# Optimization experiments

Measured on AMD Instinct MI355X. Metric: run time of the kernel, lower is better.

## Reference

```python
import jax, jax.numpy as jnp
import numpy as np

D_MODEL = 1024
HEADS = 16
D_K = D_MODEL // HEADS
D_FF = 4096
EPS = 1e-5


def _layernorm(x, gamma, beta):
    mu = jnp.mean(x, axis=-1, keepdims=True)
    var = jnp.var(x, axis=-1, keepdims=True)
    return (x - mu) * jax.lax.rsqrt(var + EPS) * gamma + beta


def setup_inputs() -> dict:
    key = jax.random.key(0)
    ks = jax.random.split(key, 8)
    s = 0.02
    return {
        "x": jax.random.normal(ks[0], (4, 2048, D_MODEL), dtype=jnp.float32),
        "wq": jax.random.normal(ks[1], (D_MODEL, D_MODEL), dtype=jnp.float32) * s,
        "wk": jax.random.normal(ks[2], (D_MODEL, D_MODEL), dtype=jnp.float32) * s,
        "wv": jax.random.normal(ks[3], (D_MODEL, D_MODEL), dtype=jnp.float32) * s,
        "wo": jax.random.normal(ks[4], (D_MODEL, D_MODEL), dtype=jnp.float32) * s,
        "w1": jax.random.normal(ks[5], (D_MODEL, D_FF), dtype=jnp.float32) * s,
        "b1": jnp.zeros((D_FF,), dtype=jnp.float32),
        "w2": jax.random.normal(ks[6], (D_FF, D_MODEL), dtype=jnp.float32) * s,
        "b2": jnp.zeros((D_MODEL,), dtype=jnp.float32),
        "g1": jnp.ones((D_MODEL,), dtype=jnp.float32),
        "be1": jnp.zeros((D_MODEL,), dtype=jnp.float32),
        "g2": jnp.ones((D_MODEL,), dtype=jnp.float32),
        "be2": jnp.zeros((D_MODEL,), dtype=jnp.float32),
    }


def reference(x, wq, wk, wv, wo, w1, b1, w2, b2, g1, be1, g2, be2):
    B, S, D = x.shape
    # --- multi-head self-attention (dropout = identity at eval) ---
    q = (x @ wq).reshape(B, S, HEADS, D_K).transpose(0, 2, 1, 3)  # [B,H,S,dk]
    k = (x @ wk).reshape(B, S, HEADS, D_K).transpose(0, 2, 1, 3)
    v = (x @ wv).reshape(B, S, HEADS, D_K).transpose(0, 2, 1, 3)
    scores = jnp.einsum("bhqd,bhkd->bhqk", q, k) / jnp.sqrt(jnp.float32(D_K))
    attn = jax.nn.softmax(scores, axis=-1)
    ctx = jnp.einsum("bhqk,bhkd->bhqd", attn, v)
    ctx = ctx.transpose(0, 2, 1, 3).reshape(B, S, D)
    attn_out = ctx @ wo
    # --- add & norm 1 ---
    h = _layernorm(x + attn_out, g1, be1)
    # --- FFN ---
    ffn = jax.nn.relu(h @ w1 + b1) @ w2 + b2
    # --- add & norm 2 ---
    return _layernorm(h + ffn, g2, be2)
```

## Files before the change

### kernel.cpp

```cpp
#include <hip/hip_runtime.h>
#include <hip/hip_bf16.h>


typedef float  floatx2  __attribute__((ext_vector_type(2)));
typedef float  floatx4  __attribute__((ext_vector_type(4)));
typedef float  floatx16 __attribute__((ext_vector_type(16)));
typedef short  shortx8  __attribute__((ext_vector_type(8)));
typedef short  shortx4  __attribute__((ext_vector_type(4)));
typedef int    intx4    __attribute__((ext_vector_type(4)));
typedef unsigned uintx2 __attribute__((ext_vector_type(2)));

__device__ __forceinline__ short f2bs(float f) {
    union { float f; unsigned u; } a; a.f = f;
    unsigned r = a.u + 0x7fffu + ((a.u >> 16) & 1u);
    return (short)(r >> 16);
}

__device__ __forceinline__ float fexp2(float x) {
#if __has_builtin(__builtin_amdgcn_exp2f)
    return __builtin_amdgcn_exp2f(x);
#else
    return __expf(0.6931471805599453f * x);
#endif
}

__device__ __forceinline__ void lane32swap(unsigned& a, unsigned& b) {
#if __has_builtin(__builtin_amdgcn_permlane32_swap)
    uintx2 r = __builtin_amdgcn_permlane32_swap(a, b, false, false);
    a = r[0]; b = r[1];
#else
    int hl = (threadIdx.x & 63) >> 5;
    unsigned ta = (unsigned)__shfl_xor((int)a, 32);
    unsigned tb = (unsigned)__shfl_xor((int)b, 32);
    unsigned na = hl ? tb : a;
    unsigned nb = hl ? b : ta;
    a = na; b = nb;
#endif
}

__device__ __forceinline__ void gload16(const short* g, short* l) {
    __builtin_amdgcn_global_load_lds(
        (const __attribute__((address_space(1))) void*)g,
        (__attribute__((address_space(3))) void*)l,
        16, 0, 0);
}

#define WAITV(n) asm volatile("s_waitcnt vmcnt(" #n ")" ::: "memory")
#define FENCE    asm volatile("" ::: "memory")

__device__ __forceinline__ void trans_tile(const float* __restrict__ in,
                                           short* __restrict__ out,
                                           int N, int K, int k0, int n0,
                                           short (*t)[68]) {
    const int tid = threadIdx.x;
    const int r = tid >> 4, c4 = (tid & 15) * 4;
#pragma unroll
    for (int i = 0; i < 4; ++i) {
        int k = r + i * 16;
        floatx4 v = *(const floatx4*)(in + (size_t)(k0 + k) * N + n0 + c4);
        shortx4 s;
#pragma unroll
        for (int j = 0; j < 4; ++j) s[j] = f2bs(v[j]);
        *(shortx4*)(&t[k][c4]) = s;
    }
    __syncthreads();
#pragma unroll
    for (int i = 0; i < 4; ++i) {
        int n = r + i * 16;
        shortx4 s;
#pragma unroll
        for (int j = 0; j < 4; ++j) s[j] = t[c4 + j][n];
        *(shortx4*)(out + (size_t)(n0 + n) * K + k0 + c4) = s;
    }
}

__global__ __launch_bounds__(256) void prep_kernel(
    const float* __restrict__ wq, const float* __restrict__ wk,
    const float* __restrict__ wv, const float* __restrict__ wo,
    const float* __restrict__ w1, const float* __restrict__ w2,
    const float* __restrict__ x,
    short* wqt, short* wkt, short* wvt, short* wot,
    short* w1t, short* w2t, short* xb)
{
    __shared__ __align__(16) short t[64][68];
    const int bid = blockIdx.x;
    if (bid < 1024) {
        const int widx = bid >> 8, local = bid & 255;
        const float* in = widx == 0 ? wq : widx == 1 ? wk : widx == 2 ? wv : wo;
        short* out = widx == 0 ? wqt : widx == 1 ? wkt : widx == 2 ? wvt : wot;
        trans_tile(in, out, 1024, 1024, (local & 15) * 64, (local >> 4) * 64, t);
    } else if (bid < 2048) {
        const int local = bid - 1024;
        trans_tile(w1, w1t, 4096, 1024, (local & 15) * 64, (local >> 4) * 64, t);
    } else if (bid < 3072) {
        const int local = bid - 2048;
        trans_tile(w2, w2t, 1024, 4096, (local & 63) * 64, (local >> 6) * 64, t);
    } else {
        const int local = bid - 3072;
#pragma unroll
        for (int j = 0; j < 4; ++j) {
            int i = local * 1024 + j * 256 + threadIdx.x;
            floatx4 v = *(const floatx4*)(x + (size_t)i * 4);
            shortx4 o;
            o[0] = f2bs(v[0]); o[1] = f2bs(v[1]); o[2] = f2bs(v[2]); o[3] = f2bs(v[3]);
            *(shortx4*)(xb + (size_t)i * 4) = o;
        }
    }
}

template<int EPI, int BN>
__global__ __launch_bounds__(512, 2) void gemm256(
    const short* __restrict__ A, const short* __restrict__ Bt, const int K, const int N,
    short* __restrict__ outb, float* __restrict__ outf,
    const float* __restrict__ bias, const float* __restrict__ resf)
{
    constexpr int BUFSZ = 16384 + BN * 64;
    constexpr int NF = BN / 64;
    __shared__ __align__(16) short Ls[2 * BUFSZ];
    const int tid = threadIdx.x;
    const int w = tid >> 6, lane = tid & 63;
    const int quad = lane >> 4, l16 = lane & 15;
    const int wm = w >> 2, wn = w & 3;
    const int bx = blockIdx.x, by = blockIdx.y;

    const int srow = w * 16 + (lane >> 3);
    const int uc0 = ((lane & 7) ^ ((lane >> 4) & 7)) * 8;
    const int uc1 = ((lane & 7) ^ (((lane >> 4) + 4) & 7)) * 8;
    const short* aS0 = A  + (size_t)(by * 256 + srow) * K + uc0;
    const short* aS1 = A  + (size_t)(by * 256 + srow + 8) * K + uc1;
    const short* bS0 = Bt + (size_t)(bx * BN + srow) * K + uc0;
    const short* bS1 = Bt + (size_t)(bx * BN + srow + 8) * K + uc1;
    const size_t hK = (size_t)128 * K;
    const int wsl = w * 1024;

    const int rswz = (l16 >> 1) & 7;
    const int ru0 = (quad ^ rswz) * 8;
    const int ru1 = ((4 + quad) ^ rswz) * 8;
    const int aRd = (wm * 64 + l16) * 64;
    const int bRd = (wn * 32 + l16) * 64;

    floatx4 acc[8][NF] = {};
    shortx8 af[4][2], blo[2][2], bhi[2][2];

#define S_A0(buf, kc) { short* p = Ls + (buf) * BUFSZ + wsl;         gload16(aS0 + (kc), p);      gload16(aS1 + (kc), p + 512);      FENCE; }
#define S_A1(buf, kc) { short* p = Ls + (buf) * BUFSZ + 8192 + wsl;  gload16(aS0 + hK + (kc), p); gload16(aS1 + hK + (kc), p + 512); FENCE; }
#define S_B0(buf, kc) { short* p = Ls + (buf) * BUFSZ + 16384 + wsl; gload16(bS0 + (kc), p);      gload16(bS1 + (kc), p + 512);      FENCE; }
#define S_B1(buf, kc) { short* p = Ls + (buf) * BUFSZ + 24576 + wsl; gload16(bS0 + hK + (kc), p); gload16(bS1 + hK + (kc), p + 512); FENCE; }
#define MF(a, b, c) c = __builtin_amdgcn_mfma_f32_16x16x32_bf16(a, b, c, 0, 0, 0)

    const int NT = K >> 6;

    if constexpr (BN == 256) {
        S_A0(0, 0) S_B0(0, 0) S_B1(0, 0) S_A1(0, 0)
        for (int t = 0; t < NT - 1; ++t) {
            const int rb = t & 1, wbuf = rb ^ 1, kc = (t + 1) * 64;
            const short* Ab = Ls + rb * BUFSZ;
            const short* Bb = Ab + 16384;
            WAITV(4); __builtin_amdgcn_s_barrier(); FENCE;
#pragma unroll
            for (int mf = 0; mf < 4; ++mf) {
                af[mf][0] = *(const shortx8*)(Ab + aRd + mf * 1024 + ru0);
                af[mf][1] = *(const shortx8*)(Ab + aRd + mf * 1024 + ru1);
            }
#pragma unroll
            for (int nf = 0; nf < 2; ++nf) {
                blo[nf][0] = *(const shortx8*)(Bb + bRd + nf * 1024 + ru0);
                blo[nf][1] = *(const shortx8*)(Bb + bRd + nf * 1024 + ru1);
            }
            S_A0(wbuf, kc)
            __builtin_amdgcn_s_setprio(1);
#pragma unroll
            for (int mf = 0; mf < 4; ++mf)
#pragma unroll
                for (int nf = 0; nf < 2; ++nf) {
                    MF(af[mf][0], blo[nf][0], acc[mf][nf]);
                    MF(af[mf][1], blo[nf][1], acc[mf][nf]);
                }
            __builtin_amdgcn_s_setprio(0);
            WAITV(4); __builtin_amdgcn_s_barrier(); FENCE;
#pragma unroll
            for (int nf = 0; nf < 2; ++nf) {
                bhi[nf][0] = *(const shortx8*)(Bb + bRd + 8192 + nf * 1024 + ru0);
                bhi[nf][1] = *(const shortx8*)(Bb + bRd + 8192 + nf * 1024 + ru1);
            }
            S_B0(wbuf, kc)
            __builtin_amdgcn_s_setprio(1);
#pragma unroll
            for (int mf = 0; mf < 4; ++mf)
#pragma unroll
                for (int nf = 0; nf < 2; ++nf) {
                    MF(af[mf][0], bhi[nf][0], acc[mf][2 + nf]);
                    MF(af[mf][1], bhi[nf][1], acc[mf][2 + nf]);
                }
            __builtin_amdgcn_s_setprio(0);
            WAITV(4); __builtin_amdgcn_s_barrier(); FENCE;
#pragma unroll
            for (int mf = 0; mf < 4; ++mf) {
                af[mf][0] = *(const shortx8*)(Ab + aRd + 8192 + mf * 1024 + ru0);
                af[mf][1] = *(const shortx8*)(Ab + aRd + 8192 + mf * 1024 + ru1);
            }
            S_B1(wbuf, kc)
            __builtin_amdgcn_s_setprio(1);
#pragma unroll
            for (int mf = 0; mf < 4; ++mf)
#pragma unroll
                for (int nf = 0; nf < 2; ++nf) {
                    MF(af[mf][0], blo[nf][0], acc[4 + mf][nf]);
                    MF(af[mf][1], blo[nf][1], acc[4 + mf][nf]);
                }
            __builtin_amdgcn_s_setprio(0);
            S_A1(wbuf, kc)
            __builtin_amdgcn_s_setprio(1);
#pragma unroll
            for (int mf = 0; mf < 4; ++mf)
#pragma unroll
                for (int nf = 0; nf < 2; ++nf) {
                    MF(af[mf][0], bhi[nf][0], acc[4 + mf][2 + nf]);
                    MF(af[mf][1], bhi[nf][1], acc[4 + mf][2 + nf]);
                }
            __builtin_amdgcn_s_setprio(0);
        }
        {
            const int rb = (NT - 1) & 1;
            const short* Ab = Ls + rb * BUFSZ;
            const short* Bb = Ab + 16384;
            WAITV(4); __builtin_amdgcn_s_barrier(); FENCE;
#pragma unroll
            for (int mf = 0; mf < 4; ++mf) {
                af[mf][0] = *(const shortx8*)(Ab + aRd + mf * 1024 + ru0);
                af[mf][1] = *(const shortx8*)(Ab + aRd + mf * 1024 + ru1);
            }
#pragma unroll
            for (int nf = 0; nf < 2; ++nf) {
                blo[nf][0] = *(const shortx8*)(Bb + bRd + nf * 1024 + ru0);
                blo[nf][1] = *(const shortx8*)(Bb + bRd + nf * 1024 + ru1);
            }
            __builtin_amdgcn_s_setprio(1);
#pragma unroll
            for (int mf = 0; mf < 4; ++mf)
#pragma unroll
                for (int nf = 0; nf < 2; ++nf) {
                    MF(af[mf][0], blo[nf][0], acc[mf][nf]);
                    MF(af[mf][1], blo[nf][1], acc[mf][nf]);
                }
            __builtin_amdgcn_s_setprio(0);
            WAITV(2); __builtin_amdgcn_s_barrier(); FENCE;
#pragma unroll
            for (int nf = 0; nf < 2; ++nf) {
                bhi[nf][0] = *(const shortx8*)(Bb + bRd + 8192 + nf * 1024 + ru0);
                bhi[nf][1] = *(const shortx8*)(Bb + bRd + 8192 + nf * 1024 + ru1);
            }
            __builtin_amdgcn_s_setprio(1);
#pragma unroll
            for (int mf = 0; mf < 4; ++mf)
#pragma unroll
                for (int nf = 0; nf < 2; ++nf) {
                    MF(af[mf][0], bhi[nf][0], acc[mf][2 + nf]);
                    MF(af[mf][1], bhi[nf][1], acc[mf][2 + nf]);
                }
            __builtin_amdgcn_s_setprio(0);
            WAITV(0); __builtin_amdgcn_s_barrier(); FENCE;
#pragma unroll
            for (int mf = 0; mf < 4; ++mf) {
                af[mf][0] = *(const shortx8*)(Ab + aRd + 8192 + mf * 1024 + ru0);
                af[mf][1] = *(const shortx8*)(Ab + aRd + 8192 + mf * 1024 + ru1);
            }
            __builtin_amdgcn_s_setprio(1);
#pragma unroll
            for (int mf = 0; mf < 4; ++mf)
#pragma unroll
                for (int nf = 0; nf < 2; ++nf) {
                    MF(af[mf][0], blo[nf][0], acc[4 + mf][nf]);
                    MF(af[mf][1], blo[nf][1], acc[4 + mf][nf]);
                    MF(af[mf][0], bhi[nf][0], acc[4 + mf][2 + nf]);
                    MF(af[mf][1], bhi[nf][1], acc[4 + mf][2 + nf]);
                }
            __builtin_amdgcn_s_setprio(0);
        }
    } else {
        S_A0(0, 0) S_B0(0, 0) S_A1(0, 0)
        for (int t = 0; t < NT - 1; ++t) {
            const int rb = t & 1, wbuf = rb ^ 1, kc = (t + 1) * 64;
            const short* Ab = Ls + rb * BUFSZ;
            const short* Bb = Ab + 16384;
            WAITV(2); __builtin_amdgcn_s_barrier(); FENCE;
#pragma unroll
            for (int mf = 0; mf < 4; ++mf) {
                af[mf][0] = *(const shortx8*)(Ab + aRd + mf * 1024 + ru0);
                af[mf][1] = *(const shortx8*)(Ab + aRd + mf * 1024 + ru1);
            }
#pragma unroll
            for (int nf = 0; nf < 2; ++nf) {
                blo[nf][0] = *(const shortx8*)(Bb + bRd + nf * 1024 + ru0);
                blo[nf][1] = *(const shortx8*)(Bb + bRd + nf * 1024 + ru1);
            }
            S_A0(wbuf, kc)
            __builtin_amdgcn_s_setprio(1);
#pragma unroll
            for (int mf = 0; mf < 4; ++mf)
#pragma unroll
                for (int nf = 0; nf < 2; ++nf) {
                    MF(af[mf][0], blo[nf][0], acc[mf][nf]);
                    MF(af[mf][1], blo[nf][1], acc[mf][nf]);
                }
            __builtin_amdgcn_s_setprio(0);
            WAITV(2); __builtin_amdgcn_s_barrier(); FENCE;
#pragma unroll
            for (int mf = 0; mf < 4; ++mf) {
                af[mf][0] = *(const shortx8*)(Ab + aRd + 8192 + mf * 1024 + ru0);
                af[mf][1] = *(const shortx8*)(Ab + aRd + 8192 + mf * 1024 + ru1);
            }
            S_B0(wbuf, kc) S_A1(wbuf, kc)
            __builtin_amdgcn_s_setprio(1);
#pragma unroll
            for (int mf = 0; mf < 4; ++mf)
#pragma unroll
                for (int nf = 0; nf < 2; ++nf) {
                    MF(af[mf][0], blo[nf][0], acc[4 + mf][nf]);
                    MF(af[mf][1], blo[nf][1], acc[4 + mf][nf]);
                }
            __builtin_amdgcn_s_setprio(0);
        }
        {
            const int rb = (NT - 1) & 1;
            const short* Ab = Ls + rb * BUFSZ;
            const short* Bb = Ab + 16384;
            WAITV(2); __builtin_amdgcn_s_barrier(); FENCE;
#pragma unroll
            for (int mf = 0; mf < 4; ++mf) {
                af[mf][0] = *(const shortx8*)(Ab + aRd + mf * 1024 + ru0);
                af[mf][1] = *(const shortx8*)(Ab + aRd + mf * 1024 + ru1);
            }
#pragma unroll
            for (int nf = 0; nf < 2; ++nf) {
                blo[nf][0] = *(const shortx8*)(Bb + bRd + nf * 1024 + ru0);
                blo[nf][1] = *(const shortx8*)(Bb + bRd + nf * 1024 + ru1);
            }
            __builtin_amdgcn_s_setprio(1);
#pragma unroll
            for (int mf = 0; mf < 4; ++mf)
#pragma unroll
                for (int nf = 0; nf < 2; ++nf) {
                    MF(af[mf][0], blo[nf][0], acc[mf][nf]);
                    MF(af[mf][1], blo[nf][1], acc[mf][nf]);
                }
            __builtin_amdgcn_s_setprio(0);
            WAITV(0); __builtin_amdgcn_s_barrier(); FENCE;
#pragma unroll
            for (int mf = 0; mf < 4; ++mf) {
                af[mf][0] = *(const shortx8*)(Ab + aRd + 8192 + mf * 1024 + ru0);
                af[mf][1] = *(const shortx8*)(Ab + aRd + 8192 + mf * 1024 + ru1);
            }
            __builtin_amdgcn_s_setprio(1);
#pragma unroll
            for (int mf = 0; mf < 4; ++mf)
#pragma unroll
                for (int nf = 0; nf < 2; ++nf) {
                    MF(af[mf][0], blo[nf][0], acc[4 + mf][nf]);
                    MF(af[mf][1], blo[nf][1], acc[4 + mf][nf]);
                }
            __builtin_amdgcn_s_setprio(0);
        }
    }

#pragma unroll
    for (int mf = 0; mf < 8; ++mf) {
        const int grow0 = by * 256 + (mf >> 2) * 128 + wm * 64 + (mf & 3) * 16 + quad * 4;
#pragma unroll
        for (int nf = 0; nf < NF; ++nf) {
            int gcol;
            if constexpr (BN == 256)
                gcol = bx * 256 + (nf >> 1) * 128 + wn * 32 + (nf & 1) * 16 + l16;
            else
                gcol = bx * 128 + wn * 32 + nf * 16 + l16;
            const floatx4 a = acc[mf][nf];
            if constexpr (EPI == 5) {
                const int slice = gcol >> 10, c = gcol & 1023;
                const int hh = c >> 6, d = c & 63;
                const int b = grow0 >> 11, s0 = grow0 & 2047;
                if (slice == 2) {
                    short* vt = outb + ((size_t)16 << 20);
                    shortx4 pkv;
#pragma unroll
                    for (int r = 0; r < 4; ++r) pkv[r] = f2bs(a[r]);
                    *(shortx4*)(vt + ((size_t)((b * 16 + hh) * 64 + d)) * 2048 + s0) = pkv;
                } else {
                    short* dst = slice ? (outb + ((size_t)8 << 20)) : outb;
                    float sc = slice ? 1.f : 0.125f * 1.4426950408889634f;
#pragma unroll
                    for (int r = 0; r < 4; ++r)
                        dst[(((size_t)(b * 16 + hh)) * 2048 + (s0 + r)) * 64 + d] =
                            f2bs(a[r] * sc);
                }
            } else if constexpr (EPI == 1) {
                const float bv = bias[gcol];
#pragma unroll
                for (int r = 0; r < 4; ++r) {
                    float v = fmaxf(a[r] + bv, 0.f);
                    outb[(size_t)(grow0 + r) * N + gcol] = f2bs(v);
                }
            } else if constexpr (EPI == 2) {
#pragma unroll
                for (int r = 0; r < 4; ++r)
                    outf[(size_t)(grow0 + r) * N + gcol] =
                        a[r] + resf[(size_t)(grow0 + r) * N + gcol];
            } else if constexpr (EPI == 3) {
                const float bv = bias[gcol];
#pragma unroll
                for (int r = 0; r < 4; ++r)
                    outf[(size_t)(grow0 + r) * N + gcol] =
                        a[r] + bv + resf[(size_t)(grow0 + r) * N + gcol];
            }
        }
    }
#undef S_A0
#undef S_A1
#undef S_B0
#undef S_B1
#undef MF
}

__global__ __launch_bounds__(256) void ln_kernel(
    const float* __restrict__ in, float* __restrict__ outf, short* __restrict__ outb,
    const float* __restrict__ g, const float* __restrict__ be, int writeB)
{
    __shared__ float red[8];
    const int row = blockIdx.x, tid = threadIdx.x;
    const float* p = in + (size_t)row * 1024;
    floatx4 v = *(const floatx4*)(p + tid * 4);
    float s = v[0] + v[1] + v[2] + v[3];
    float q = v[0] * v[0] + v[1] * v[1] + v[2] * v[2] + v[3] * v[3];
#pragma unroll
    for (int off = 32; off; off >>= 1) {
        s += __shfl_xor(s, off);
        q += __shfl_xor(q, off);
    }
    int w = tid >> 6, lane = tid & 63;
    if (lane == 0) { red[w] = s; red[4 + w] = q; }
    __syncthreads();
    s = red[0] + red[1] + red[2] + red[3];
    q = red[4] + red[5] + red[6] + red[7];
    float mean = s * (1.f / 1024.f);
    float var = q * (1.f / 1024.f) - mean * mean;
    float rs = rsqrtf(var + 1e-5f);
    floatx4 gv = *(const floatx4*)(g + tid * 4);
    floatx4 bv = *(const floatx4*)(be + tid * 4);
    floatx4 o4;
#pragma unroll
    for (int i = 0; i < 4; ++i) o4[i] = (v[i] - mean) * rs * gv[i] + bv[i];
    *(floatx4*)(outf + (size_t)row * 1024 + tid * 4) = o4;
    if (writeB) {
        shortx4 ob;
#pragma unroll
        for (int i = 0; i < 4; ++i) ob[i] = f2bs(o4[i]);
        *(shortx4*)(outb + (size_t)row * 1024 + tid * 4) = ob;
    }
}

__global__ __launch_bounds__(256) void attn_kernel(
    const short* __restrict__ Q, const short* __restrict__ K,
    const short* __restrict__ Vt, short* __restrict__ ctx)
{
    __shared__ __align__(16) short Ks[128 * 72];
    __shared__ __align__(16) short Vs[64 * 136];
    const int tid = threadIdx.x;
    const int q0 = blockIdx.x * 128, bh = blockIdx.y;
    const int w = tid >> 6, lane = tid & 63, l31 = lane & 31, hl = lane >> 5;
    const size_t sb = (size_t)bh * 2048 * 64;

    shortx8 qf[4];
#pragma unroll
    for (int ks = 0; ks < 4; ++ks)
        qf[ks] = *(const shortx8*)(Q + sb + (size_t)(q0 + w * 32 + l31) * 64 + ks * 16 + hl * 8);

    const int krow = tid >> 3, kcol = (tid & 7) * 8;
    const int vrow = tid >> 4, vcol = (tid & 15) * 8;

    floatx16 o[2] = {};
    floatx2 rsA = {0.f, 0.f}, rsB = {0.f, 0.f};
    const floatx16 z = {};

    intx4 kv[4], vv[4];
#pragma unroll
    for (int i = 0; i < 4; ++i) {
        kv[i] = *(const intx4*)(K + sb + (size_t)(i * 32 + krow) * 64 + kcol);
        vv[i] = *(const intx4*)(Vt + sb + (size_t)(i * 16 + vrow) * 2048 + vcol);
    }

#define LD_AK(mt, ks) (*(const shortx8*)(Ks + ((mt) * 32 + l31) * 72 + (ks) * 16 + hl * 8))
#define LD_AV(mtd, mt, ksl) (*(const shortx8*)(Vs + ((mtd) * 32 + l31) * 136 + (mt) * 32 + (ksl) * 16 + hl * 8))

    for (int kt = 0; kt < 16; ++kt) {
        __syncthreads();
#pragma unroll
        for (int i = 0; i < 4; ++i) {
            *(intx4*)(Ks + (i * 32 + krow) * 72 + kcol) = kv[i];
            *(intx4*)(Vs + (i * 16 + vrow) * 136 + vcol) = vv[i];
        }
        __syncthreads();
        if (kt < 15) {
            const int kv0 = (kt + 1) * 128;
#pragma unroll
            for (int i = 0; i < 4; ++i) {
                kv[i] = *(const intx4*)(K + sb + (size_t)(kv0 + i * 32 + krow) * 64 + kcol);
                vv[i] = *(const intx4*)(Vt + sb + (size_t)(i * 16 + vrow) * 2048 + kv0 + vcol);
            }
        }

        floatx16 sc;
        {
            __builtin_amdgcn_s_setprio(1);
            sc = __builtin_amdgcn_mfma_f32_32x32x16_bf16(LD_AK(0, 0), qf[0], z, 0, 0, 0);
            sc = __builtin_amdgcn_mfma_f32_32x32x16_bf16(LD_AK(0, 1), qf[1], sc, 0, 0, 0);
            sc = __builtin_amdgcn_mfma_f32_32x32x16_bf16(LD_AK(0, 2), qf[2], sc, 0, 0, 0);
            sc = __builtin_amdgcn_mfma_f32_32x32x16_bf16(LD_AK(0, 3), qf[3], sc, 0, 0, 0);
            __builtin_amdgcn_s_setprio(0);
        }
#pragma unroll
        for (int mt = 0; mt < 4; ++mt) {
            floatx16 sn;
            if (mt < 3) {
                __builtin_amdgcn_s_setprio(1);
                sn = __builtin_amdgcn_mfma_f32_32x32x16_bf16(LD_AK(mt + 1, 0), qf[0], z, 0, 0, 0);
                sn = __builtin_amdgcn_mfma_f32_32x32x16_bf16(LD_AK(mt + 1, 1), qf[1], sn, 0, 0, 0);
                sn = __builtin_amdgcn_mfma_f32_32x32x16_bf16(LD_AK(mt + 1, 2), qf[2], sn, 0, 0, 0);
                sn = __builtin_amdgcn_mfma_f32_32x32x16_bf16(LD_AK(mt + 1, 3), qf[3], sn, 0, 0, 0);
                __builtin_amdgcn_s_setprio(0);
            }
            floatx2 ps2[8];
#pragma unroll
            for (int i = 0; i < 8; ++i) {
                ps2[i][0] = fexp2(sc[2 * i]);
                ps2[i][1] = fexp2(sc[2 * i + 1]);
            }
#pragma unroll
            for (int i = 0; i < 8; i += 2) { rsA += ps2[i]; rsB += ps2[i + 1]; }
            unsigned pk[8];
#pragma unroll
            for (int i = 0; i < 8; ++i) {
                union { __hip_bfloat162 h; unsigned u; } cv;
                cv.h = __float22bfloat162_rn(make_float2(ps2[i][0], ps2[i][1]));
                pk[i] = cv.u;
            }
            lane32swap(pk[0], pk[2]);
            lane32swap(pk[1], pk[3]);
            lane32swap(pk[4], pk[6]);
            lane32swap(pk[5], pk[7]);
            __builtin_amdgcn_s_setprio(1);
#pragma unroll
            for (int ksl = 0; ksl < 2; ++ksl) {
                union { unsigned i[4]; shortx8 s8; } fr;
                fr.i[0] = pk[4 * ksl];     fr.i[1] = pk[4 * ksl + 1];
                fr.i[2] = pk[4 * ksl + 2]; fr.i[3] = pk[4 * ksl + 3];
#pragma unroll
                for (int mtd = 0; mtd < 2; ++mtd)
                    o[mtd] = __builtin_amdgcn_mfma_f32_32x32x16_bf16(LD_AV(mtd, mt, ksl), fr.s8, o[mtd], 0, 0, 0);
            }
            __builtin_amdgcn_s_setprio(0);
            if (mt < 3) sc = sn;
        }
    }
#undef LD_AK
#undef LD_AV

    float rsum = rsA[0] + rsA[1] + rsB[0] + rsB[1];
    float tot = rsum + __shfl_xor(rsum, 32);
    float inv = 1.f / tot;

    __syncthreads();
    short* O_lds = Ks;
#pragma unroll
    for (int mtd = 0; mtd < 2; ++mtd)
#pragma unroll
        for (int g = 0; g < 4; ++g) {
            shortx4 p4;
#pragma unroll
            for (int r = 0; r < 4; ++r) p4[r] = f2bs(o[mtd][4 * g + r] * inv);
            *(shortx4*)(O_lds + (w * 32 + l31) * 72 + mtd * 32 + g * 8 + hl * 4) = p4;
        }
    __syncthreads();
    const int b = bh >> 4, head = bh & 15;
#pragma unroll
    for (int it = 0; it < 4; ++it) {
        int idx = it * 256 + tid;
        int q = idx >> 3, ch = idx & 7;
        shortx8 v = *(const shortx8*)(O_lds + q * 72 + ch * 8);
        *(shortx8*)(ctx + ((size_t)(b * 2048 + q0 + q)) * 1024 + head * 64 + ch * 8) = v;
    }
}

extern "C" void kernel_launch(void* const* d_in, const int* in_sizes, int n_in,
                              void* d_out, int out_size, void* d_ws, size_t ws_size,
                              hipStream_t stream) {
    const float* x   = (const float*)d_in[0];
    const float* wq  = (const float*)d_in[1];
    const float* wk  = (const float*)d_in[2];
    const float* wv  = (const float*)d_in[3];
    const float* wo  = (const float*)d_in[4];
    const float* w1  = (const float*)d_in[5];
    const float* b1  = (const float*)d_in[6];
    const float* w2  = (const float*)d_in[7];
    const float* b2  = (const float*)d_in[8];
    const float* g1p = (const float*)d_in[9];
    const float* be1 = (const float*)d_in[10];
    const float* g2p = (const float*)d_in[11];
    const float* be2 = (const float*)d_in[12];
    float* out = (float*)d_out;

    char* ws = (char*)d_ws;
    const size_t MB = 1ull << 20;
    short* wqt  = (short*)(ws + 0 * MB);
    short* wkt  = (short*)(ws + 2 * MB);
    short* wvt  = (short*)(ws + 4 * MB);
    short* wot  = (short*)(ws + 6 * MB);
    short* w1t  = (short*)(ws + 8 * MB);
    short* w2t  = (short*)(ws + 16 * MB);
    short* xb   = (short*)(ws + 24 * MB);
    short* Qb   = (short*)(ws + 40 * MB);
    short* Kb   = (short*)(ws + 56 * MB);
    short* Vtg  = (short*)(ws + 72 * MB);
    short* ctxb = (short*)(ws + 88 * MB);
    float* tf   = (float*)(ws + 104 * MB);
    short* hb   = (short*)(ws + 136 * MB);
    short* f1b  = (short*)(ws + 40 * MB);

    prep_kernel<<<5120, 256, 0, stream>>>(wq, wk, wv, wo, w1, w2, x,
                                          wqt, wkt, wvt, wot, w1t, w2t, xb);

    gemm256<5, 128><<<dim3(24, 32), 512, 0, stream>>>(xb, wqt, 1024, 3072, Qb, nullptr, nullptr, nullptr);
    attn_kernel<<<dim3(16, 64), 256, 0, stream>>>(Qb, Kb, Vtg, ctxb);
    gemm256<2, 128><<<dim3(8, 32), 512, 0, stream>>>(ctxb, wot, 1024, 1024, nullptr, tf, nullptr, x);
    ln_kernel<<<8192, 256, 0, stream>>>(tf, tf, hb, g1p, be1, 1);
    gemm256<1, 256><<<dim3(16, 32), 512, 0, stream>>>(hb, w1t, 1024, 4096, f1b, nullptr, b1, nullptr);
    gemm256<3, 128><<<dim3(8, 32), 512, 0, stream>>>(f1b, w2t, 4096, 1024, nullptr, out, b2, tf);
    ln_kernel<<<8192, 256, 0, stream>>>(out, out, nullptr, g2p, be2, 0);
}
```

Baseline: 410.5 us.

## Load K/V tiles directly to LDS with XOR swizzle in attention kernel

Replaces the register-staged K/V prefetch (global->VGPR->LDS with padded rows) with direct global-to-LDS 16-byte loads (gload16) into unpadded tiles. Bank conflicts are avoided with an XOR swizzle of the column chunk index. The kernel also drops the software-pipelined score MFMA (sn/sc double buffering) and sets launch_bounds min-blocks to 4, which lowers register use to raise occupancy. The cost is that each tile is now loaded synchronously (WAITV(0) before the barrier) with no prefetch overlap. The kernel relies on more resident waves to hide that latency.

```diff
diff --git a/kernel.cpp b/kernel.cpp
--- a/kernel.cpp
+++ b/kernel.cpp
@@ -457,12 +457,13 @@
     }
 }
 
-__global__ __launch_bounds__(256) void attn_kernel(
+__global__ __launch_bounds__(256, 4) void attn_kernel(
     const short* __restrict__ Q, const short* __restrict__ K,
     const short* __restrict__ Vt, short* __restrict__ ctx)
 {
-    __shared__ __align__(16) short Ks[128 * 72];
-    __shared__ __align__(16) short Vs[64 * 136];
+    __shared__ __align__(16) short Ls[16384];
+    short* Ks = Ls;
+    short* Vs = Ls + 8192;
     const int tid = threadIdx.x;
     const int q0 = blockIdx.x * 128, bh = blockIdx.y;
     const int w = tid >> 6, lane = tid & 63, l31 = lane & 31, hl = lane >> 5;
@@ -473,60 +474,45 @@
     for (int ks = 0; ks < 4; ++ks)
         qf[ks] = *(const shortx8*)(Q + sb + (size_t)(q0 + w * 32 + l31) * 64 + ks * 16 + hl * 8);
 
-    const int krow = tid >> 3, kcol = (tid & 7) * 8;
-    const int vrow = tid >> 4, vcol = (tid & 15) * 8;
+    const short* kSrc = K + sb + (size_t)(w * 32 + (lane >> 3)) * 64
+                        + (((lane & 7) ^ ((lane >> 3) & 7)) * 8);
+    int vOff[4];
+#pragma unroll
+    for (int j = 0; j < 4; ++j)
+        vOff[j] = (w * 16 + j * 4 + (lane >> 4)) * 2048
+                  + (((lane & 15) ^ (j * 4 + (lane >> 4))) * 8);
+    const short* vBase = Vt + sb;
+
+    const int kx = l31 & 7, vx = l31 & 15;
 
     floatx16 o[2] = {};
     floatx2 rsA = {0.f, 0.f}, rsB = {0.f, 0.f};
     const floatx16 z = {};
 
-    intx4 kv[4], vv[4];
-#pragma unroll
-    for (int i = 0; i < 4; ++i) {
-        kv[i] = *(const intx4*)(K + sb + (size_t)(i * 32 + krow) * 64 + kcol);
-        vv[i] = *(const intx4*)(Vt + sb + (size_t)(i * 16 + vrow) * 2048 + vcol);
-    }
-
-#define LD_AK(mt, ks) (*(const shortx8*)(Ks + ((mt) * 32 + l31) * 72 + (ks) * 16 + hl * 8))
-#define LD_AV(mtd, mt, ksl) (*(const shortx8*)(Vs + ((mtd) * 32 + l31) * 136 + (mt) * 32 + (ksl) * 16 + hl * 8))
+#define LD_AK(mt, ks) (*(const shortx8*)(Ks + ((mt) * 32 + l31) * 64 + ((((ks) * 2 + hl) ^ kx)) * 8))
+#define LD_AV(mtd, mt, ksl) (*(const shortx8*)(Vs + ((mtd) * 32 + l31) * 128 + ((((mt) * 4 + (ksl) * 2 + hl) ^ vx)) * 8))
 
     for (int kt = 0; kt < 16; ++kt) {
+        const int kv0 = kt * 128;
         __syncthreads();
 #pragma unroll
-        for (int i = 0; i < 4; ++i) {
-            *(intx4*)(Ks + (i * 32 + krow) * 72 + kcol) = kv[i];
-            *(intx4*)(Vs + (i * 16 + vrow) * 136 + vcol) = vv[i];
-        }
+        for (int j = 0; j < 4; ++j)
+            gload16(kSrc + (size_t)kv0 * 64 + j * 512, Ks + (w * 4 + j) * 512);
+#pragma unroll
+        for (int j = 0; j < 4; ++j)
+            gload16(vBase + vOff[j] + kv0, Vs + (w * 4 + j) * 512);
+        WAITV(0);
         __syncthreads();
-        if (kt < 15) {
-            const int kv0 = (kt + 1) * 128;
-#pragma unroll
-            for (int i = 0; i < 4; ++i) {
-                kv[i] = *(const intx4*)(K + sb + (size_t)(kv0 + i * 32 + krow) * 64 + kcol);
-                vv[i] = *(const intx4*)(Vt + sb + (size_t)(i * 16 + vrow) * 2048 + kv0 + vcol);
-            }
-        }
-
-        floatx16 sc;
-        {
-            __builtin_amdgcn_s_setprio(1);
-            sc = __builtin_amdgcn_mfma_f32_32x32x16_bf16(LD_AK(0, 0), qf[0], z, 0, 0, 0);
-            sc = __builtin_amdgcn_mfma_f32_32x32x16_bf16(LD_AK(0, 1), qf[1], sc, 0, 0, 0);
-            sc = __builtin_amdgcn_mfma_f32_32x32x16_bf16(LD_AK(0, 2), qf[2], sc, 0, 0, 0);
-            sc = __builtin_amdgcn_mfma_f32_32x32x16_bf16(LD_AK(0, 3), qf[3], sc, 0, 0, 0);
-            __builtin_amdgcn_s_setprio(0);
-        }
+
 #pragma unroll
         for (int mt = 0; mt < 4; ++mt) {
-            floatx16 sn;
-            if (mt < 3) {
-                __builtin_amdgcn_s_setprio(1);
-                sn = __builtin_amdgcn_mfma_f32_32x32x16_bf16(LD_AK(mt + 1, 0), qf[0], z, 0, 0, 0);
-                sn = __builtin_amdgcn_mfma_f32_32x32x16_bf16(LD_AK(mt + 1, 1), qf[1], sn, 0, 0, 0);
-                sn = __builtin_amdgcn_mfma_f32_32x32x16_bf16(LD_AK(mt + 1, 2), qf[2], sn, 0, 0, 0);
-                sn = __builtin_amdgcn_mfma_f32_32x32x16_bf16(LD_AK(mt + 1, 3), qf[3], sn, 0, 0, 0);
-                __builtin_amdgcn_s_setprio(0);
-            }
+            floatx16 sc;
+            __builtin_amdgcn_s_setprio(1);
+            sc = __builtin_amdgcn_mfma_f32_32x32x16_bf16(LD_AK(mt, 0), qf[0], z, 0, 0, 0);
+            sc = __builtin_amdgcn_mfma_f32_32x32x16_bf16(LD_AK(mt, 1), qf[1], sc, 0, 0, 0);
+            sc = __builtin_amdgcn_mfma_f32_32x32x16_bf16(LD_AK(mt, 2), qf[2], sc, 0, 0, 0);
+            sc = __builtin_amdgcn_mfma_f32_32x32x16_bf16(LD_AK(mt, 3), qf[3], sc, 0, 0, 0);
+            __builtin_amdgcn_s_setprio(0);
             floatx2 ps2[8];
 #pragma unroll
             for (int i = 0; i < 8; ++i) {
@@ -557,7 +543,6 @@
                     o[mtd] = __builtin_amdgcn_mfma_f32_32x32x16_bf16(LD_AV(mtd, mt, ksl), fr.s8, o[mtd], 0, 0, 0);
             }
             __builtin_amdgcn_s_setprio(0);
-            if (mt < 3) sc = sn;
         }
     }
 #undef LD_AK
@@ -568,7 +553,7 @@
     float inv = 1.f / tot;
 
     __syncthreads();
-    short* O_lds = Ks;
+    short* O_lds = Ls;
 #pragma unroll
     for (int mtd = 0; mtd < 2; ++mtd)
 #pragma unroll
```

Result: faster. 395.9 us (-3.6%).
